# Performance work log

Hardware: AMD Instinct MI355X
Metric: run time of the kernel (lower is better)

The kernel has to match this reference:

```python
import jax, jax.numpy as jnp
import numpy as np

B, CDD, HIS, T, L, D, K = 64, 5, 100, 30, 3, 256, 10
THRESHOLD = 0.1


def setup_inputs() -> dict:
    key = jax.random.key(0)
    k1, k2, k3, k4 = jax.random.split(key, 4)
    cdd_repr = jax.random.normal(k1, (B, CDD, D), dtype=jnp.float32)
    his_repr = jax.random.normal(k2, (B, HIS, D), dtype=jnp.float32)
    his_embedding = jax.random.normal(k3, (B, HIS, T, L, D), dtype=jnp.float32)
    # xavier_normal init for Linear(D, D)
    W_sel = jax.random.normal(k4, (D, D), dtype=jnp.float32) * np.sqrt(2.0 / (D + D))
    b_sel = jnp.zeros((D,), dtype=jnp.float32)
    return {"cdd_repr": cdd_repr, "his_repr": his_repr,
            "his_embedding": his_embedding, "W_sel": W_sel, "b_sel": b_sel}


def _l2_normalize(x, eps=1e-12):
    # matches torch F.normalize(dim=-1)
    n = jnp.linalg.norm(x, axis=-1, keepdims=True)
    return x / jnp.maximum(n, eps)


def reference(cdd_repr, his_repr, his_embedding, W_sel, b_sel):
    # selectionProject (Linear) + L2 normalize
    cdd_p = _l2_normalize(cdd_repr @ W_sel.T + b_sel)   # [B, CDD, D]
    his_p = _l2_normalize(his_repr @ W_sel.T + b_sel)   # [B, HIS, D]

    # news-level attention scores [B, CDD, HIS]
    attn = jnp.einsum('bcd,bhd->bch', cdd_p, his_p)

    # top-k over history
    attn_topk, idx = jax.lax.top_k(attn, K)             # [B, CDD, K]

    # multi-dim gather of history embeddings -> [B, CDD, K, T, L, D]
    his_activated = his_embedding[jnp.arange(B)[:, None, None], idx]

    # threshold masking: zero out weights below threshold, scale embeddings
    w = jnp.where(attn_topk < THRESHOLD, 0.0, attn_topk)
    his_activated = his_activated * w[:, :, :, None, None, None]

    return his_activated, idx
```

## Files before the change

kernel.cpp:

```cpp
#include <hip/hip_runtime.h>
#include <hip/hip_bf16.h>

#define NB   64
#define NCDD 5
#define NHIS 100
#define ND   256
#define NK   10
#define TLD  23040
#define THRESH 0.1f
#define NEG_INF (-3.402823466e38f)

typedef float f32x4 __attribute__((ext_vector_type(4)));

__global__ __launch_bounds__(256) void proj_norm_kernel(
    const float* __restrict__ X,
    const float* __restrict__ W,
    const float* __restrict__ bvec,
    float* __restrict__ Y)
{
    __shared__ float xs[16][256];
    __shared__ float red[4][16];
    const int r0  = blockIdx.x * 16;
    const int tid = threadIdx.x;

    for (int i = tid; i < 16 * 64; i += 256) {
        const int row = i >> 6, c4 = i & 63;
        ((float4*)&xs[row][0])[c4] =
            ((const float4*)(X + (size_t)(r0 + row) * ND))[c4];
    }
    __syncthreads();

    const int d = tid;
    const float bias = bvec[d];
    float acc[16];
#pragma unroll
    for (int r = 0; r < 16; ++r) acc[r] = bias;

    const float* wrow = W + (size_t)d * ND;
    for (int k = 0; k < ND; k += 4) {
        const float4 w4 = *(const float4*)(wrow + k);
#pragma unroll
        for (int r = 0; r < 16; ++r) {
            const float4 x4 = *(const float4*)&xs[r][k];
            acc[r] += w4.x * x4.x + w4.y * x4.y + w4.z * x4.z + w4.w * x4.w;
        }
    }

    const int wave = tid >> 6, lane = tid & 63;
#pragma unroll
    for (int r = 0; r < 16; ++r) {
        float v = acc[r] * acc[r];
        for (int off = 32; off; off >>= 1) v += __shfl_xor(v, off);
        if (lane == 0) red[wave][r] = v;
    }
    __syncthreads();

#pragma unroll
    for (int r = 0; r < 16; ++r) {
        const float s = red[0][r] + red[1][r] + red[2][r] + red[3][r];
        const float scale = 1.0f / fmaxf(sqrtf(s), 1e-12f);
        Y[(size_t)(r0 + r) * ND + d] = acc[r] * scale;
    }
}

__global__ __launch_bounds__(256) void cdd_attn_topk_kernel(
    const float* __restrict__ cdd_repr,
    const float* __restrict__ W,
    const float* __restrict__ bvec,
    const float* __restrict__ his_p,
    float* __restrict__ out_idx_f,
    int* __restrict__ ws_idx,
    float* __restrict__ ws_w)
{
    __shared__ float xs[ND];
    __shared__ float cvec[ND];
    __shared__ float attn_s[NHIS];
    __shared__ float red[4];
    const int bc  = blockIdx.x;
    const int b   = bc / NCDD;
    const int tid = threadIdx.x;
    const int wave = tid >> 6, lane = tid & 63;

    xs[tid] = cdd_repr[(size_t)bc * ND + tid];
    __syncthreads();

    float acc = bvec[tid];
    const float* wrow = W + (size_t)tid * ND;
    for (int k = 0; k < ND; k += 4) {
        const float4 w4 = *(const float4*)(wrow + k);
        const float4 x4 = *(const float4*)&xs[k];
        acc += w4.x * x4.x + w4.y * x4.y + w4.z * x4.z + w4.w * x4.w;
    }
    float ss = acc * acc;
    for (int off = 32; off; off >>= 1) ss += __shfl_xor(ss, off);
    if (lane == 0) red[wave] = ss;
    __syncthreads();
    const float s = red[0] + red[1] + red[2] + red[3];
    const float scale = 1.0f / fmaxf(sqrtf(s), 1e-12f);
    cvec[tid] = acc * scale;
    __syncthreads();

    const float4 c4 = ((const float4*)cvec)[lane];
    for (int h = wave; h < NHIS; h += 4) {
        const float4 h4 =
            ((const float4*)(his_p + ((size_t)b * NHIS + h) * ND))[lane];
        float v = c4.x * h4.x + c4.y * h4.y + c4.z * h4.z + c4.w * h4.w;
        for (int off = 32; off; off >>= 1) v += __shfl_xor(v, off);
        if (lane == 0) attn_s[h] = v;
    }
    __syncthreads();

    if (wave == 0) {
        float v0 = attn_s[lane];
        float v1 = (lane + 64 < NHIS) ? attn_s[lane + 64] : NEG_INF;
#pragma unroll
        for (int k = 0; k < NK; ++k) {
            float lv; int li;
            if (v1 > v0) { lv = v1; li = lane + 64; }
            else         { lv = v0; li = lane; }
            for (int off = 1; off < 64; off <<= 1) {
                const float ov = __shfl_xor(lv, off);
                const int   oi = __shfl_xor(li, off);
                if (ov > lv || (ov == lv && oi < li)) { lv = ov; li = oi; }
            }
            if (lane == 0) {
                const float w = (lv < THRESH) ? 0.0f : lv;
                const int g = bc * NK + k;
                ws_idx[g] = li;
                ws_w[g]   = w;
                out_idx_f[g] = (float)li;
            }
            if (li == lane)            v0 = NEG_INF;
            else if (li == lane + 64)  v1 = NEG_INF;
        }
    }
}

__global__ __launch_bounds__(256) void gather_kernel(
    const float* __restrict__ his_emb,
    const int* __restrict__ ws_idx,
    const float* __restrict__ ws_w,
    float* __restrict__ out)
{
    const int g = blockIdx.x;
    const int b = g / (NCDD * NK);
    const int idx = ws_idx[g];
    const float w = ws_w[g];
    const int tid = threadIdx.x;

    const f32x4* __restrict__ src =
        (const f32x4*)(his_emb + ((size_t)b * NHIS + idx) * TLD);
    f32x4* __restrict__ dst = (f32x4*)(out + (size_t)g * TLD);

#pragma unroll 4
    for (int it = 0; it < 22; ++it) {
        const int i = tid + it * 256;
        f32x4 v = src[i];
        v *= w;
        __builtin_nontemporal_store(v, dst + i);
    }
    if (tid < 128) {
        const int i = 22 * 256 + tid;
        f32x4 v = src[i];
        v *= w;
        __builtin_nontemporal_store(v, dst + i);
    }
}

extern "C" void kernel_launch(void* const* d_in, const int* in_sizes, int n_in,
                              void* d_out, int out_size, void* d_ws, size_t ws_size,
                              hipStream_t stream)
{
    const float* cdd_repr = (const float*)d_in[0];
    const float* his_repr = (const float*)d_in[1];
    const float* his_emb  = (const float*)d_in[2];
    const float* W_sel    = (const float*)d_in[3];
    const float* b_sel    = (const float*)d_in[4];
    float* out = (float*)d_out;

    char* ws = (char*)d_ws;
    float* his_p = (float*)(ws);
    int*   idx_i = (int*)  (ws + 6553600);
    float* w_w   = (float*)(ws + 6566400);

    float* out_idx_f = out + (size_t)NB * NCDD * NK * TLD;

    proj_norm_kernel<<<(NB * NHIS) / 16, 256, 0, stream>>>(his_repr, W_sel, b_sel, his_p);
    cdd_attn_topk_kernel<<<NB * NCDD, 256, 0, stream>>>(cdd_repr, W_sel, b_sel,
                                                        his_p, out_idx_f, idx_i, w_w);
    gather_kernel<<<NB * NCDD * NK, 256, 0, stream>>>(his_emb, idx_i, w_w, out);
}
```

Baseline: 179.3 us.

## Skip source reads for zero-weight gathers, remap blocks, drop LDS staging

The gather kernel now writes zeros directly when the top-k weight is below threshold, so no history embedding is read for those blocks. Block indices are remapped across 8 strided groups, likely to spread work across XCDs or memory channels. The projection kernels also stop staging inputs in shared memory and read them straight from global memory through the cache. Skipping the read is exact, because the output is multiplied by zero anyway, apart from NaN or Inf values in the source. The benefit depends on how many top-k scores fall below the threshold.

```diff
diff --git a/kernel.cpp b/kernel.cpp
--- a/kernel.cpp
+++ b/kernel.cpp
@@ -18,30 +18,21 @@
     const float* __restrict__ bvec,
     float* __restrict__ Y)
 {
-    __shared__ float xs[16][256];
     __shared__ float red[4][16];
     const int r0  = blockIdx.x * 16;
     const int tid = threadIdx.x;
 
-    for (int i = tid; i < 16 * 64; i += 256) {
-        const int row = i >> 6, c4 = i & 63;
-        ((float4*)&xs[row][0])[c4] =
-            ((const float4*)(X + (size_t)(r0 + row) * ND))[c4];
-    }
-    __syncthreads();
-
-    const int d = tid;
-    const float bias = bvec[d];
+    const float bias = bvec[tid];
     float acc[16];
 #pragma unroll
     for (int r = 0; r < 16; ++r) acc[r] = bias;
 
-    const float* wrow = W + (size_t)d * ND;
+    const float* wrow = W + (size_t)tid * ND;
     for (int k = 0; k < ND; k += 4) {
         const float4 w4 = *(const float4*)(wrow + k);
 #pragma unroll
         for (int r = 0; r < 16; ++r) {
-            const float4 x4 = *(const float4*)&xs[r][k];
+            const float4 x4 = *(const float4*)(X + (size_t)(r0 + r) * ND + k);
             acc[r] += w4.x * x4.x + w4.y * x4.y + w4.z * x4.z + w4.w * x4.w;
         }
     }
@@ -59,7 +50,7 @@
     for (int r = 0; r < 16; ++r) {
         const float s = red[0][r] + red[1][r] + red[2][r] + red[3][r];
         const float scale = 1.0f / fmaxf(sqrtf(s), 1e-12f);
-        Y[(size_t)(r0 + r) * ND + d] = acc[r] * scale;
+        Y[(size_t)(r0 + r) * ND + tid] = acc[r] * scale;
     }
 }
 
@@ -72,7 +63,6 @@
     int* __restrict__ ws_idx,
     float* __restrict__ ws_w)
 {
-    __shared__ float xs[ND];
     __shared__ float cvec[ND];
     __shared__ float attn_s[NHIS];
     __shared__ float red[4];
@@ -81,14 +71,12 @@
     const int tid = threadIdx.x;
     const int wave = tid >> 6, lane = tid & 63;
 
-    xs[tid] = cdd_repr[(size_t)bc * ND + tid];
-    __syncthreads();
-
     float acc = bvec[tid];
     const float* wrow = W + (size_t)tid * ND;
+    const float* xrow = cdd_repr + (size_t)bc * ND;
     for (int k = 0; k < ND; k += 4) {
         const float4 w4 = *(const float4*)(wrow + k);
-        const float4 x4 = *(const float4*)&xs[k];
+        const float4 x4 = *(const float4*)(xrow + k);
         acc += w4.x * x4.x + w4.y * x4.y + w4.z * x4.z + w4.w * x4.w;
     }
     float ss = acc * acc;
@@ -142,15 +130,27 @@
     const float* __restrict__ ws_w,
     float* __restrict__ out)
 {
-    const int g = blockIdx.x;
+    const int orig = blockIdx.x;
+    const int g = (orig & 7) * 400 + (orig >> 3);
     const int b = g / (NCDD * NK);
+    const int tid = threadIdx.x;
+    const float w = ws_w[g];
+
+    f32x4* __restrict__ dst = (f32x4*)(out + (size_t)g * TLD);
+
+    if (w == 0.0f) {
+        const f32x4 z = {0.f, 0.f, 0.f, 0.f};
+#pragma unroll
+        for (int it = 0; it < 22; ++it)
+            __builtin_nontemporal_store(z, dst + tid + it * 256);
+        if (tid < 128)
+            __builtin_nontemporal_store(z, dst + 22 * 256 + tid);
+        return;
+    }
+
     const int idx = ws_idx[g];
-    const float w = ws_w[g];
-    const int tid = threadIdx.x;
-
     const f32x4* __restrict__ src =
         (const f32x4*)(his_emb + ((size_t)b * NHIS + idx) * TLD);
-    f32x4* __restrict__ dst = (f32x4*)(out + (size_t)g * TLD);
 
 #pragma unroll 4
     for (int it = 0; it < 22; ++it) {
```

Measured after the change: 179.2 us. No clear change (-0.1%).
